# Kernel tuning notes

Hardware: AMD Instinct MI355X
Metric: run time of the kernel (lower is better)

## Reference

```python
import jax, jax.numpy as jnp
import numpy as np

B, S, D = 16, 1024, 1024      # batch, seq_len (== max_ctx_k), input_dim (== embed_dim)
H = 1                          # num_heads (module's v-reshape requires 1)
E = 1024                       # embed_dim
TEMP = 1.0
EPS = 1e-12


def setup_inputs() -> dict:
    key = jax.random.key(0)
    ks = jax.random.split(key, 10)
    x = jax.random.normal(ks[0], (B, S, D), dtype=jnp.float32)
    mask = jax.random.randint(ks[1], (B, S, S), 0, 2, dtype=jnp.int32)
    # parameters (xavier-ish scales)
    Wqkv = jax.random.normal(ks[2], (2 * E, D), dtype=jnp.float32) * (1.0 / np.sqrt(D))
    bqkv = jax.random.normal(ks[3], (2 * E,), dtype=jnp.float32) * 0.02
    Wctx = jax.random.normal(ks[4], (2 * S, S), dtype=jnp.float32) * (1.0 / np.sqrt(S))
    bctx = jax.random.normal(ks[5], (2 * S,), dtype=jnp.float32) * 0.02
    Wf = jax.random.normal(ks[6], (1, 2), dtype=jnp.float32)
    bf = jax.random.normal(ks[7], (1,), dtype=jnp.float32) * 0.02
    Wo = jax.random.normal(ks[8], (D, 2 * D), dtype=jnp.float32) * (1.0 / np.sqrt(2 * D))
    bo = jax.random.normal(ks[9], (D,), dtype=jnp.float32) * 0.02
    return {"x": x, "mask": mask, "Wqkv": Wqkv, "bqkv": bqkv, "Wctx": Wctx,
            "bctx": bctx, "Wf": Wf, "bf": bf, "Wo": Wo, "bo": bo}


def reference(x, mask, Wqkv, bqkv, Wctx, bctx, Wf, bf, Wo, bo):
    head_dim = E // H
    # qkv projection -> (B, H, S, 2*head_dim)
    qkv = (jnp.einsum('bsd,ed->bse', x, Wqkv) + bqkv)
    qkv = qkv.reshape(B, S, H, 2 * head_dim).transpose(0, 2, 1, 3)
    q, k = jnp.split(qkv, 2, axis=-1)
    # v is just x per head (num_heads == 1)
    v = x.reshape(B, S, H, D).transpose(0, 2, 1, 3)          # (B, H, S, D)
    # self-attention scores (NOT scaled by sqrt(d_k), faithful to source)
    self_attn = jnp.einsum('bhqd,bhkd->bhqk', q, k)           # (B, H, S, S)
    # adjacency-derived context scores
    adj = jnp.einsum('bqd,bkd->bqk', x, x)[:, None]           # (B, 1, S, S)
    ctx_qk = jnp.einsum('bhqs,ts->bhqt', adj, Wctx) + bctx    # (B, 1, S, 2S)
    ctx_q, ctx_k = jnp.split(ctx_qk, 2, axis=-1)
    ctx_q = ctx_q / jnp.maximum(jnp.linalg.norm(ctx_q, axis=-1, keepdims=True), EPS)
    ctx_k = ctx_k / jnp.maximum(jnp.linalg.norm(ctx_k, axis=-1, keepdims=True), EPS)
    ctx_attn = jnp.einsum('bhqs,bhks->bhqk', ctx_q, ctx_k)    # (B, 1, S, S)
    # learned fuse of the two score maps: Linear(2 -> 1)
    attn = self_attn * Wf[0, 0] + ctx_attn * Wf[0, 1] + bf[0]
    attn = jax.nn.softmax(attn / TEMP, axis=-1)
    # post-softmax masking + L1 renorm
    m = (mask[:, None] != 0)                                  # (B, 1, S, S)
    attn = jnp.where(m, attn, 0.0)
    attn = attn / jnp.maximum(jnp.sum(jnp.abs(attn), axis=-1, keepdims=True), EPS)
    # value matmul and output projection
    values = jnp.einsum('bhqk,bhkd->bhqd', attn, v)           # (B, H, S, D)
    values = values.transpose(0, 2, 1, 3).reshape(B, S, D)
    o = jnp.einsum('bse,de->bsd', jnp.concatenate([x, values], axis=-1), Wo) + bo
    return o
```

## Files before the change

kernel.cpp:

```cpp
#include <hip/hip_runtime.h>
#include <hip/hip_bf16.h>

#define BB 16
#define SS 1024
#define DD 1024

typedef __hip_bfloat16 bf;
using s8v   = __attribute__((ext_vector_type(8))) short;
using f32x4 = __attribute__((ext_vector_type(4))) float;
using u16x4 = __attribute__((ext_vector_type(4))) unsigned short;
using u16x8 = __attribute__((ext_vector_type(8))) unsigned short;
using i32x4 = __attribute__((ext_vector_type(4))) int;

__device__ __forceinline__ void gload16(const bf* g, unsigned short* l)
{
    __builtin_amdgcn_global_load_lds(
        (const __attribute__((address_space(1))) void*)g,
        (__attribute__((address_space(3))) void*)l,
        16, 0, 0);
}

template <int EP>
__global__ __launch_bounds__(512, 2) void gemm256(
    const bf* __restrict__ A, long sA, int lda, int segA,
    const bf* __restrict__ B, long sB, int ldb, int segB,
    float* __restrict__ C, bf* __restrict__ Cb,
    bf* __restrict__ qp, bf* __restrict__ kp,
    long sC, int ldc, int K,
    const float* __restrict__ bias,
    const float* __restrict__ alpha_ptr, int alpha_idx,
    const float* __restrict__ addc_ptr,
    int accumulate)
{
    __shared__ __align__(16) unsigned short lds[65536];
    unsigned short* Asm = lds;
    unsigned short* Bsm = lds + 32768;

    const int gx = gridDim.x, gy = gridDim.y;
    const int nwg = gx * gy * (int)gridDim.z;
    int lid = blockIdx.x + gx * (blockIdx.y + gy * blockIdx.z);
    lid = (lid & 7) * (nwg >> 3) + (lid >> 3);
    const int bx = lid % gx;
    const int rem = lid / gx;
    const int by = rem % gy;
    const int bz = rem / gy;

    const int tid = threadIdx.x;
    const int w = tid >> 6, l = tid & 63;
    const int wm = w >> 2, wn = w & 3;
    const int lm = l & 15, quad = l >> 4;
    const int bh = wn >> 1;
    const int bl0 = (wn & 1) * 64;

    const int m0 = by * 256, n0 = bx * 256;
    const bf* Ab = A + (long)bz * sA;
    const bf* Bb = B + (long)bz * sB;

    const int srow = w * 16 + (l >> 3);
    const int scol = ((l & 7) ^ (l >> 3)) << 3;
    const long aoff0 = (long)srow * lda + scol;
    const long aoff1 = (long)(srow + 8) * lda + scol;
    const long boff0 = (long)srow * ldb + scol;
    const long boff1 = (long)(srow + 8) * ldb + scol;
    const int ldst = w * 1024;

    auto stageA = [&](int tt, int h) {
        const int kk = ((tt & 15) << 6) +
                       ((((unsigned)segA >> ((tt >> 4) << 3)) & 0xffu) << 10);
        const bf* g = Ab + (long)(m0 + h * 128) * lda + kk;
        unsigned short* d = Asm + (((tt & 1) << 1) + h) * 8192 + ldst;
        gload16(g + aoff0, d);
        gload16(g + aoff1, d + 512);
    };
    auto stageB = [&](int tt, int h) {
        const int kk = ((tt & 15) << 6) +
                       ((((unsigned)segB >> ((tt >> 4) << 3)) & 0xffu) << 10);
        const bf* g = Bb + (long)(n0 + h * 128) * ldb + kk;
        unsigned short* d = Bsm + (((tt & 1) << 1) + h) * 8192 + ldst;
        gload16(g + boff0, d);
        gload16(g + boff1, d + 512);
    };
    auto rdA = [&](int d, int rl, int ks) -> s8v {
        const int off = rl * 64 + (((ks << 5) + (quad << 3)) ^ ((rl & 7) << 3));
        return *(const s8v*)(Asm + ((d << 1) + wm) * 8192 + off);
    };
    auto rdB = [&](int d, int bl, int ks) -> s8v {
        const int off = bl * 64 + (((ks << 5) + (quad << 3)) ^ ((bl & 7) << 3));
        return *(const s8v*)(Bsm + ((d << 1) + bh) * 8192 + off);
    };

    f32x4 acc[8][4];
#pragma unroll
    for (int i = 0; i < 8; ++i)
#pragma unroll
        for (int j = 0; j < 4; ++j)
            acc[i][j] = (f32x4){0.f, 0.f, 0.f, 0.f};

    const int NT = K >> 6;

    stageA(0, 0); stageA(0, 1); stageB(0, 0); stageB(0, 1);
    asm volatile("s_waitcnt vmcnt(4)" ::: "memory");
    stageA(1, 0); stageA(1, 1); stageB(1, 0);
    asm volatile("s_waitcnt vmcnt(6)" ::: "memory");
    __builtin_amdgcn_s_barrier();

    s8v a[8], b[4];
    for (int t = 0; t < NT; ++t) {
        const int d = t & 1;
#pragma unroll
        for (int mf = 0; mf < 4; ++mf) {
            a[mf * 2]     = rdA(d, mf * 16 + lm, 0);
            a[mf * 2 + 1] = rdA(d, mf * 16 + lm, 1);
        }
#pragma unroll
        for (int nf = 0; nf < 2; ++nf) {
            b[nf * 2]     = rdB(d, bl0 + nf * 16 + lm, 0);
            b[nf * 2 + 1] = rdB(d, bl0 + nf * 16 + lm, 1);
        }
        if (t + 1 < NT) stageB(t + 1, 1);
        __builtin_amdgcn_s_barrier();
        __builtin_amdgcn_s_setprio(1);
#pragma unroll
        for (int mf = 0; mf < 4; ++mf)
#pragma unroll
            for (int nf = 0; nf < 2; ++nf) {
                acc[mf][nf] = __builtin_amdgcn_mfma_f32_16x16x32_bf16(a[mf*2],   b[nf*2],   acc[mf][nf], 0, 0, 0);
                acc[mf][nf] = __builtin_amdgcn_mfma_f32_16x16x32_bf16(a[mf*2+1], b[nf*2+1], acc[mf][nf], 0, 0, 0);
            }
        __builtin_amdgcn_s_setprio(0);
        __builtin_amdgcn_s_barrier();
#pragma unroll
        for (int nf = 0; nf < 2; ++nf) {
            b[nf * 2]     = rdB(d, bl0 + (nf + 2) * 16 + lm, 0);
            b[nf * 2 + 1] = rdB(d, bl0 + (nf + 2) * 16 + lm, 1);
        }
        __builtin_amdgcn_s_barrier();
        __builtin_amdgcn_s_setprio(1);
#pragma unroll
        for (int mf = 0; mf < 4; ++mf)
#pragma unroll
            for (int nf = 0; nf < 2; ++nf) {
                acc[mf][nf+2] = __builtin_amdgcn_mfma_f32_16x16x32_bf16(a[mf*2],   b[nf*2],   acc[mf][nf+2], 0, 0, 0);
                acc[mf][nf+2] = __builtin_amdgcn_mfma_f32_16x16x32_bf16(a[mf*2+1], b[nf*2+1], acc[mf][nf+2], 0, 0, 0);
            }
        __builtin_amdgcn_s_setprio(0);
        __builtin_amdgcn_s_barrier();
#pragma unroll
        for (int mf = 0; mf < 4; ++mf) {
            a[mf * 2]     = rdA(d, 64 + mf * 16 + lm, 0);
            a[mf * 2 + 1] = rdA(d, 64 + mf * 16 + lm, 1);
        }
        if (t + 2 < NT) { stageA(t + 2, 0); stageA(t + 2, 1); }
        __builtin_amdgcn_s_barrier();
        __builtin_amdgcn_s_setprio(1);
#pragma unroll
        for (int mf = 0; mf < 4; ++mf)
#pragma unroll
            for (int nf = 0; nf < 2; ++nf) {
                acc[mf+4][nf+2] = __builtin_amdgcn_mfma_f32_16x16x32_bf16(a[mf*2],   b[nf*2],   acc[mf+4][nf+2], 0, 0, 0);
                acc[mf+4][nf+2] = __builtin_amdgcn_mfma_f32_16x16x32_bf16(a[mf*2+1], b[nf*2+1], acc[mf+4][nf+2], 0, 0, 0);
            }
        __builtin_amdgcn_s_setprio(0);
        __builtin_amdgcn_s_barrier();
#pragma unroll
        for (int nf = 0; nf < 2; ++nf) {
            b[nf * 2]     = rdB(d, bl0 + nf * 16 + lm, 0);
            b[nf * 2 + 1] = rdB(d, bl0 + nf * 16 + lm, 1);
        }
        if (t + 2 < NT) {
            stageB(t + 2, 0);
            asm volatile("s_waitcnt vmcnt(6)" ::: "memory");
        } else {
            asm volatile("s_waitcnt vmcnt(0)" ::: "memory");
        }
        __builtin_amdgcn_s_barrier();
        __builtin_amdgcn_s_setprio(1);
#pragma unroll
        for (int mf = 0; mf < 4; ++mf)
#pragma unroll
            for (int nf = 0; nf < 2; ++nf) {
                acc[mf+4][nf] = __builtin_amdgcn_mfma_f32_16x16x32_bf16(a[mf*2],   b[nf*2],   acc[mf+4][nf], 0, 0, 0);
                acc[mf+4][nf] = __builtin_amdgcn_mfma_f32_16x16x32_bf16(a[mf*2+1], b[nf*2+1], acc[mf+4][nf], 0, 0, 0);
            }
        __builtin_amdgcn_s_setprio(0);
        __builtin_amdgcn_s_barrier();
    }

    const float alpha = alpha_ptr ? alpha_ptr[alpha_idx] : 1.0f;
    const float addc  = addc_ptr ? addc_ptr[0] : 0.0f;
    float* Cp = C ? C + (long)bz * sC : nullptr;
    bf* Cbp = (EP == 1) ? Cb + (long)bz * sC : nullptr;
    bf* qpz = (EP == 2 || EP == 3) ? qp + (long)bz * sC : nullptr;
    bf* kpz = (EP == 2 || EP == 3) ? kp + (long)bz * sC : nullptr;

#pragma unroll
    for (int mf = 0; mf < 8; ++mf) {
#pragma unroll
        for (int nf = 0; nf < 4; ++nf) {
            const int cidx = n0 + wn * 64 + nf * 16 + lm;
            const float bv = bias ? bias[cidx] : 0.0f;
            const long rbase = m0 + wm * 128 + mf * 16 + quad * 4;
#pragma unroll
            for (int r = 0; r < 4; ++r) {
                const long row = rbase + r;
                if (EP == 2) {
                    float v = acc[mf][nf][r] + bv;
                    if (cidx < 1024) {
                        v *= alpha;
                        bf hi = __float2bfloat16(v);
                        bf lo = __float2bfloat16(v - __bfloat162float(hi));
                        qpz[row * 3072 + cidx] = hi;
                        qpz[row * 3072 + 1024 + cidx] = lo;
                    } else {
                        const int c = cidx - 1024;
                        bf hi = __float2bfloat16(v);
                        bf lo = __float2bfloat16(v - __bfloat162float(hi));
                        kpz[row * 3072 + c] = hi;
                        kpz[row * 3072 + 1024 + c] = lo;
                    }
                } else if (EP == 3) {
                    const float v = acc[mf][nf][r] + bv;
                    const bf h = __float2bfloat16(v);
                    if (cidx < 1024) qpz[row * 3072 + 2048 + cidx] = h;
                    else             kpz[row * 3072 + 2048 + (cidx - 1024)] = h;
                } else {
                    float v = alpha * acc[mf][nf][r] + addc + bv;
                    const long off = row * (long)ldc + cidx;
                    if (EP == 1) {
                        Cbp[off] = __float2bfloat16(v);
                    } else {
                        if (accumulate) v += Cp[off];
                        Cp[off] = v;
                    }
                }
            }
        }
    }
}

__device__ inline float blockReduceSum(float v, float* red)
{
#pragma unroll
    for (int off = 32; off > 0; off >>= 1) v += __shfl_xor(v, off, 64);
    __syncthreads();
    if ((threadIdx.x & 63) == 0) red[threadIdx.x >> 6] = v;
    __syncthreads();
    return red[0] + red[1] + red[2] + red[3];
}

__device__ inline float blockReduceMax(float v, float* red)
{
#pragma unroll
    for (int off = 32; off > 0; off >>= 1) v = fmaxf(v, __shfl_xor(v, off, 64));
    __syncthreads();
    if ((threadIdx.x & 63) == 0) red[threadIdx.x >> 6] = v;
    __syncthreads();
    return fmaxf(fmaxf(red[0], red[1]), fmaxf(red[2], red[3]));
}

__device__ inline void split_bf16(float v, bf& hi, bf& lo)
{
    hi = __float2bfloat16(v);
    lo = __float2bfloat16(v - __bfloat162float(hi));
}

__device__ __forceinline__ unsigned short bf_bits(float v)
{
    bf h = __float2bfloat16(v);
    return *reinterpret_cast<unsigned short*>(&h);
}

__global__ __launch_bounds__(256) void prep_wqkv_kernel(
    const float* __restrict__ W, bf* __restrict__ wq2)
{
    const long i4 = ((long)blockIdx.x * 256 + threadIdx.x) * 4;
    const long r = i4 >> 10; const int c = (int)(i4 & 1023);
    const f32x4 s = *(const f32x4*)&W[i4];
    u16x4 h4, l4;
#pragma unroll
    for (int j = 0; j < 4; ++j) {
        bf hi, lo; split_bf16(s[j], hi, lo);
        h4[j] = *reinterpret_cast<unsigned short*>(&hi);
        l4[j] = *reinterpret_cast<unsigned short*>(&lo);
    }
    *(u16x4*)&wq2[r * 2048 + c] = h4;
    *(u16x4*)&wq2[r * 2048 + 1024 + c] = l4;
}

__global__ __launch_bounds__(256) void conv_kernel(
    const float* __restrict__ src, bf* __restrict__ dst, int cols, int src_ld, long n)
{
    const long i4 = ((long)blockIdx.x * 256 + threadIdx.x) * 4;
    if (i4 >= n) return;
    const long r = i4 / cols; const int c = (int)(i4 % cols);
    const f32x4 s = *(const f32x4*)&src[r * src_ld + c];
    u16x4 d4;
#pragma unroll
    for (int j = 0; j < 4; ++j) d4[j] = bf_bits(s[j]);
    *(u16x4*)&dst[i4] = d4;
}

__global__ __launch_bounds__(256) void conv_x_kernel(
    const float* __restrict__ x, bf* __restrict__ xhl, bf* __restrict__ xT1)
{
    __shared__ float t[64][65];
    const int b = blockIdx.z;
    const int c0 = blockIdx.x * 64, r0 = blockIdx.y * 64;
    const int tx = threadIdx.x & 7, ty = threadIdx.x >> 3;
    const float* xb = x + (long)b * SS * DD;
    bf* xhlb = xhl + (long)b * SS * 2048;
#pragma unroll
    for (int p = 0; p < 2; ++p) {
        const int r = ty + 32 * p;
        const f32x4 v0 = *(const f32x4*)&xb[(long)(r0 + r) * DD + c0 + tx * 8];
        const f32x4 v1 = *(const f32x4*)&xb[(long)(r0 + r) * DD + c0 + tx * 8 + 4];
        u16x8 hv, lv;
#pragma unroll
        for (int j = 0; j < 4; ++j) {
            bf hi, lo;
            split_bf16(v0[j], hi, lo);
            hv[j] = *reinterpret_cast<unsigned short*>(&hi);
            lv[j] = *reinterpret_cast<unsigned short*>(&lo);
            t[r][tx * 8 + j] = v0[j];
            split_bf16(v1[j], hi, lo);
            hv[j + 4] = *reinterpret_cast<unsigned short*>(&hi);
            lv[j + 4] = *reinterpret_cast<unsigned short*>(&lo);
            t[r][tx * 8 + 4 + j] = v1[j];
        }
        *(u16x8*)&xhlb[(long)(r0 + r) * 2048 + c0 + tx * 8] = hv;
        *(u16x8*)&xhlb[(long)(r0 + r) * 2048 + 1024 + c0 + tx * 8] = lv;
    }
    __syncthreads();
#pragma unroll
    for (int p = 0; p < 2; ++p) {
        const int dd = ty + 32 * p;
        u16x8 o;
#pragma unroll
        for (int j = 0; j < 8; ++j) o[j] = bf_bits(t[tx * 8 + j][dd]);
        *(u16x8*)&xT1[(long)b * DD * SS + (long)(c0 + dd) * SS + r0 + tx * 8] = o;
    }
}

__global__ __launch_bounds__(256) void l2norm_fuse_kernel(
    bf* __restrict__ q3, bf* __restrict__ k3, const float* __restrict__ Wf)
{
    __shared__ float red[4];
    const long row = blockIdx.x >> 1;
    const int half = blockIdx.x & 1;
    bf* p = (half ? k3 : q3) + row * 3072 + 2048;
    const int t = threadIdx.x;

    const u16x4 u = *reinterpret_cast<const u16x4*>(p + 4 * t);
    float v[4];
    float ss = 0.0f;
#pragma unroll
    for (int i = 0; i < 4; ++i) {
        unsigned short us = u[i];
        v[i] = __bfloat162float(*reinterpret_cast<const bf*>(&us));
        ss = fmaf(v[i], v[i], ss);
    }
    ss = blockReduceSum(ss, red);
    const float inv = 1.0f / fmaxf(sqrtf(ss), 1e-12f);
    const float scale = half ? inv : inv * Wf[1];
    u16x4 o;
#pragma unroll
    for (int i = 0; i < 4; ++i) o[i] = bf_bits(v[i] * scale);
    *reinterpret_cast<u16x4*>(p + 4 * t) = o;
}

__global__ __launch_bounds__(256) void softmax_mask_kernel(
    const float* __restrict__ attn, const int* __restrict__ mask, bf* __restrict__ attn_bf)
{
    __shared__ float red[4];
    const long row = blockIdx.x;
    const int t4 = threadIdx.x * 4;
    const f32x4 v = *(const f32x4*)(attn + row * SS + t4);
    const i32x4 mv = *(const i32x4*)(mask + row * SS + t4);
    bf* o = attn_bf + row * SS;

    float mx = fmaxf(fmaxf(v[0], v[1]), fmaxf(v[2], v[3]));
    mx = blockReduceMax(mx, red);

    float e[4];
    float s = 0.0f;
#pragma unroll
    for (int i = 0; i < 4; ++i) { e[i] = expf(v[i] - mx); s += e[i]; }
    s = blockReduceSum(s, red);

    float l1 = 0.0f;
#pragma unroll
    for (int i = 0; i < 4; ++i) { e[i] = mv[i] ? e[i] / s : 0.0f; l1 += e[i]; }
    l1 = blockReduceSum(l1, red);
    const float inv = 1.0f / fmaxf(l1, 1e-12f);
    u16x4 ov;
#pragma unroll
    for (int i = 0; i < 4; ++i) ov[i] = bf_bits(e[i] * inv);
    *(u16x4*)(o + t4) = ov;
}

extern "C" void kernel_launch(void* const* d_in, const int* in_sizes, int n_in,
                              void* d_out, int out_size, void* d_ws, size_t ws_size,
                              hipStream_t stream)
{
    const float* x    = (const float*)d_in[0];
    const int*   mask = (const int*)d_in[1];
    const float* Wqkv = (const float*)d_in[2];
    const float* bqkv = (const float*)d_in[3];
    const float* Wctx = (const float*)d_in[4];
    const float* bctx = (const float*)d_in[5];
    const float* Wf   = (const float*)d_in[6];
    const float* bfp  = (const float*)d_in[7];
    const float* Wo   = (const float*)d_in[8];
    const float* bo   = (const float*)d_in[9];
    float* out = (float*)d_out;

    const long SD = (long)SS * DD;

    auto align_up = [](size_t v) { return (v + 255) & ~(size_t)255; };

    const size_t sz_wq2  = 2048L * 2048 * 2;
    const size_t sz_wctx = 2048L * 1024 * 2;
    const size_t sz_wob  = 1024L * 2048 * 2;
    const size_t SH = align_up(sz_wq2) + align_up(sz_wctx) + align_up(sz_wob);

    const size_t szXL = 1024L * 2048 * 2;
    const size_t szXT = 1024L * 1024 * 2;
    const size_t szQ3 = 1024L * 3072 * 2;
    const size_t szY  = 1024L * 1024 * 4;
    const size_t PB = align_up(szXL) + align_up(szXT) + 2 * align_up(szQ3) +
                      align_up(szY);

    int G = 16;
    while (G > 1 && SH + (size_t)G * PB > ws_size) G >>= 1;

    char* p = (char*)d_ws;
    auto take = [&](size_t bytes) { char* r = p; p += align_up(bytes); return r; };
    bf* Wq2   = (bf*)take(sz_wq2);
    bf* Wctx1 = (bf*)take(sz_wctx);
    bf* Wob   = (bf*)take(sz_wob);
    char* RX = take((size_t)G * szXL);
    char* RT = take((size_t)G * szXT);
    char* RQ = take((size_t)G * szQ3);
    char* RK = take((size_t)G * szQ3);
    char* RY = take((size_t)G * szY);

    bf*    xhl   = (bf*)RX;
    bf*    xT1   = (bf*)RT;
    bf*    Q3    = (bf*)RQ;
    bf*    K3    = (bf*)RK;
    bf*    adjb  = (bf*)RY;
    float* attn  = (float*)RY;
    bf*    attnb = (bf*)RQ;

    const dim3 blk(256);
    const dim3 blk5(512);
    const long sXL = 1024L * 2048;
    const long sAT = 1024L * 1024;
    const long sQ3 = 1024L * 3072;

    const int segQKV_A = 0x0100;
    const int segQKV_B = 0x010000;
    const int segATT_A = 0x02010000;
    const int segATT_B = 0x02000100;
    const int segOUT   = 0x0100;

    prep_wqkv_kernel<<<dim3((2048L * 1024) / 1024), blk, 0, stream>>>(Wqkv, Wq2);
    conv_kernel<<<dim3((2048L * 1024) / 1024), blk, 0, stream>>>(Wctx, Wctx1, 1024, 1024, 2048L * 1024);
    conv_kernel<<<dim3((1024L * 2048) / 1024), blk, 0, stream>>>(Wo, Wob, 2048, 2048, 1024L * 2048);

    for (int bc0 = 0; bc0 < BB; bc0 += G) {
        const float* xb = x + (long)bc0 * SD;
        const int M = G * 1024;

        conv_x_kernel<<<dim3(16, 16, G), blk, 0, stream>>>(xb, xhl, xT1);

        gemm256<2><<<dim3(2048 / 256, M / 256), blk5, 0, stream>>>(
            xhl, 0, 2048, segQKV_A, Wq2, 0, 2048, segQKV_B,
            nullptr, nullptr, Q3, K3, 0, 0, 3072,
            bqkv, Wf, 0, nullptr, 0);

        gemm256<1><<<dim3(1024 / 256, 1024 / 256, G), blk5, 0, stream>>>(
            xhl, sXL, 2048, 0, xhl, sXL, 2048, 0,
            nullptr, adjb, nullptr, nullptr, sAT, 1024, 1024,
            nullptr, nullptr, 0, nullptr, 0);

        gemm256<3><<<dim3(2048 / 256, 1024 / 256, G), blk5, 0, stream>>>(
            adjb, sAT, 1024, 0, Wctx1, 0, 1024, 0,
            nullptr, nullptr, Q3, K3, sQ3, 0, 1024,
            bctx, nullptr, 0, nullptr, 0);

        l2norm_fuse_kernel<<<dim3(G * 1024 * 2), blk, 0, stream>>>(Q3, K3, Wf);

        gemm256<0><<<dim3(1024 / 256, 1024 / 256, G), blk5, 0, stream>>>(
            Q3, sQ3, 3072, segATT_A, K3, sQ3, 3072, segATT_B,
            attn, nullptr, nullptr, nullptr, sAT, 1024, 4096,
            nullptr, nullptr, 0, bfp, 0);

        softmax_mask_kernel<<<dim3(G * 1024), blk, 0, stream>>>(
            attn, mask + (long)bc0 * SS * SS, attnb);

        gemm256<1><<<dim3(1024 / 256, 1024 / 256, G), blk5, 0, stream>>>(
            attnb, sAT, 1024, 0, xT1, sAT, 1024, 0,
            nullptr, xhl + 1024, nullptr, nullptr, sXL, 2048, 1024,
            nullptr, nullptr, 0, nullptr, 0);

        gemm256<0><<<dim3(1024 / 256, M / 256), blk5, 0, stream>>>(
            xhl, 0, 2048, segOUT, Wob, 0, 2048, segOUT,
            out + (long)bc0 * SD, nullptr, nullptr, nullptr, 0, 1024, 2048,
            bo, nullptr, 0, nullptr, 0);
    }
}
```

Baseline: 1.004 ms.

## Load GEMM B fragments directly from global into registers, halving LDS use

The B operand is no longer staged through shared memory. Each wave loads its own B fragments straight from global memory into double-buffered registers (bA/bB), and the tile loop is restructured into two unrolled halves with fewer barriers. This removes the LDS traffic and synchronisation for B and halves the shared-memory footprint, which could allow more occupancy. In exchange, every wave re-reads B from global or L2 with no sharing across waves, and register pressure rises from holding 16 extra B vectors.

```diff
diff --git a/kernel.cpp b/kernel.cpp
--- a/kernel.cpp
+++ b/kernel.cpp
@@ -32,9 +32,7 @@
     const float* __restrict__ addc_ptr,
     int accumulate)
 {
-    __shared__ __align__(16) unsigned short lds[65536];
-    unsigned short* Asm = lds;
-    unsigned short* Bsm = lds + 32768;
+    __shared__ __align__(16) unsigned short Asm[32768];
 
     const int gx = gridDim.x, gy = gridDim.y;
     const int nwg = gx * gy * (int)gridDim.z;
@@ -49,8 +47,6 @@
     const int w = tid >> 6, l = tid & 63;
     const int wm = w >> 2, wn = w & 3;
     const int lm = l & 15, quad = l >> 4;
-    const int bh = wn >> 1;
-    const int bl0 = (wn & 1) * 64;
 
     const int m0 = by * 256, n0 = bx * 256;
     const bf* Ab = A + (long)bz * sA;
@@ -60,8 +56,6 @@
     const int scol = ((l & 7) ^ (l >> 3)) << 3;
     const long aoff0 = (long)srow * lda + scol;
     const long aoff1 = (long)(srow + 8) * lda + scol;
-    const long boff0 = (long)srow * ldb + scol;
-    const long boff1 = (long)(srow + 8) * ldb + scol;
     const int ldst = w * 1024;
 
     auto stageA = [&](int tt, int h) {
@@ -72,21 +66,20 @@
         gload16(g + aoff0, d);
         gload16(g + aoff1, d + 512);
     };
-    auto stageB = [&](int tt, int h) {
-        const int kk = ((tt & 15) << 6) +
-                       ((((unsigned)segB >> ((tt >> 4) << 3)) & 0xffu) << 10);
-        const bf* g = Bb + (long)(n0 + h * 128) * ldb + kk;
-        unsigned short* d = Bsm + (((tt & 1) << 1) + h) * 8192 + ldst;
-        gload16(g + boff0, d);
-        gload16(g + boff1, d + 512);
-    };
     auto rdA = [&](int d, int rl, int ks) -> s8v {
         const int off = rl * 64 + (((ks << 5) + (quad << 3)) ^ ((rl & 7) << 3));
         return *(const s8v*)(Asm + ((d << 1) + wm) * 8192 + off);
     };
-    auto rdB = [&](int d, int bl, int ks) -> s8v {
-        const int off = bl * 64 + (((ks << 5) + (quad << 3)) ^ ((bl & 7) << 3));
-        return *(const s8v*)(Bsm + ((d << 1) + bh) * 8192 + off);
+    const bf* Bw = Bb + (long)(n0 + wn * 64 + lm) * ldb + quad * 8;
+    auto loadB = [&](int tt, s8v* dst) {
+        const int kk = ((tt & 15) << 6) +
+                       ((((unsigned)segB >> ((tt >> 4) << 3)) & 0xffu) << 10);
+#pragma unroll
+        for (int nf = 0; nf < 4; ++nf)
+#pragma unroll
+            for (int ks = 0; ks < 2; ++ks)
+                dst[nf * 2 + ks] =
+                    *(const s8v*)&Bw[(long)(nf * 16) * ldb + kk + ks * 32];
     };
 
     f32x4 acc[8][4];
@@ -97,51 +90,30 @@
             acc[i][j] = (f32x4){0.f, 0.f, 0.f, 0.f};
 
     const int NT = K >> 6;
-
-    stageA(0, 0); stageA(0, 1); stageB(0, 0); stageB(0, 1);
-    asm volatile("s_waitcnt vmcnt(4)" ::: "memory");
-    stageA(1, 0); stageA(1, 1); stageB(1, 0);
-    asm volatile("s_waitcnt vmcnt(6)" ::: "memory");
+    s8v bA[8], bB[8];
+
+    stageA(0, 0); stageA(0, 1);
+    loadB(0, bA);
+    stageA(1, 0); stageA(1, 1);
+    asm volatile("s_waitcnt vmcnt(12)" ::: "memory");
     __builtin_amdgcn_s_barrier();
 
-    s8v a[8], b[4];
-    for (int t = 0; t < NT; ++t) {
+    auto tile = [&](int t, s8v* bc, s8v* bn) {
         const int d = t & 1;
+        s8v a[8];
 #pragma unroll
         for (int mf = 0; mf < 4; ++mf) {
             a[mf * 2]     = rdA(d, mf * 16 + lm, 0);
             a[mf * 2 + 1] = rdA(d, mf * 16 + lm, 1);
         }
-#pragma unroll
-        for (int nf = 0; nf < 2; ++nf) {
-            b[nf * 2]     = rdB(d, bl0 + nf * 16 + lm, 0);
-            b[nf * 2 + 1] = rdB(d, bl0 + nf * 16 + lm, 1);
-        }
-        if (t + 1 < NT) stageB(t + 1, 1);
-        __builtin_amdgcn_s_barrier();
+        if (t + 1 < NT) loadB(t + 1, bn);
         __builtin_amdgcn_s_setprio(1);
 #pragma unroll
         for (int mf = 0; mf < 4; ++mf)
 #pragma unroll
-            for (int nf = 0; nf < 2; ++nf) {
-                acc[mf][nf] = __builtin_amdgcn_mfma_f32_16x16x32_bf16(a[mf*2],   b[nf*2],   acc[mf][nf], 0, 0, 0);
-                acc[mf][nf] = __builtin_amdgcn_mfma_f32_16x16x32_bf16(a[mf*2+1], b[nf*2+1], acc[mf][nf], 0, 0, 0);
-            }
-        __builtin_amdgcn_s_setprio(0);
-        __builtin_amdgcn_s_barrier();
-#pragma unroll
-        for (int nf = 0; nf < 2; ++nf) {
-            b[nf * 2]     = rdB(d, bl0 + (nf + 2) * 16 + lm, 0);
-            b[nf * 2 + 1] = rdB(d, bl0 + (nf + 2) * 16 + lm, 1);
-        }
-        __builtin_amdgcn_s_barrier();
-        __builtin_amdgcn_s_setprio(1);
-#pragma unroll
-        for (int mf = 0; mf < 4; ++mf)
-#pragma unroll
-            for (int nf = 0; nf < 2; ++nf) {
-                acc[mf][nf+2] = __builtin_amdgcn_mfma_f32_16x16x32_bf16(a[mf*2],   b[nf*2],   acc[mf][nf+2], 0, 0, 0);
-                acc[mf][nf+2] = __builtin_amdgcn_mfma_f32_16x16x32_bf16(a[mf*2+1], b[nf*2+1], acc[mf][nf+2], 0, 0, 0);
+            for (int nf = 0; nf < 4; ++nf) {
+                acc[mf][nf] = __builtin_amdgcn_mfma_f32_16x16x32_bf16(a[mf*2],   bc[nf*2],   acc[mf][nf], 0, 0, 0);
+                acc[mf][nf] = __builtin_amdgcn_mfma_f32_16x16x32_bf16(a[mf*2+1], bc[nf*2+1], acc[mf][nf], 0, 0, 0);
             }
         __builtin_amdgcn_s_setprio(0);
         __builtin_amdgcn_s_barrier();
@@ -151,39 +123,27 @@
             a[mf * 2 + 1] = rdA(d, 64 + mf * 16 + lm, 1);
         }
         if (t + 2 < NT) { stageA(t + 2, 0); stageA(t + 2, 1); }
-        __builtin_amdgcn_s_barrier();
         __builtin_amdgcn_s_setprio(1);
 #pragma unroll
         for (int mf = 0; mf < 4; ++mf)
 #pragma unroll
-            for (int nf = 0; nf < 2; ++nf) {
-                acc[mf+4][nf+2] = __builtin_amdgcn_mfma_f32_16x16x32_bf16(a[mf*2],   b[nf*2],   acc[mf+4][nf+2], 0, 0, 0);
-                acc[mf+4][nf+2] = __builtin_amdgcn_mfma_f32_16x16x32_bf16(a[mf*2+1], b[nf*2+1], acc[mf+4][nf+2], 0, 0, 0);
+            for (int nf = 0; nf < 4; ++nf) {
+                acc[mf+4][nf] = __builtin_amdgcn_mfma_f32_16x16x32_bf16(a[mf*2],   bc[nf*2],   acc[mf+4][nf], 0, 0, 0);
+                acc[mf+4][nf] = __builtin_amdgcn_mfma_f32_16x16x32_bf16(a[mf*2+1], bc[nf*2+1], acc[mf+4][nf], 0, 0, 0);
             }
         __builtin_amdgcn_s_setprio(0);
-        __builtin_amdgcn_s_barrier();
-#pragma unroll
-        for (int nf = 0; nf < 2; ++nf) {
-            b[nf * 2]     = rdB(d, bl0 + nf * 16 + lm, 0);
-            b[nf * 2 + 1] = rdB(d, bl0 + nf * 16 + lm, 1);
+        if (t + 1 < NT) {
+            if (t + 2 < NT)
+                asm volatile("s_waitcnt vmcnt(12)" ::: "memory");
+            else
+                asm volatile("s_waitcnt vmcnt(8)" ::: "memory");
+            __builtin_amdgcn_s_barrier();
         }
-        if (t + 2 < NT) {
-            stageB(t + 2, 0);
-            asm volatile("s_waitcnt vmcnt(6)" ::: "memory");
-        } else {
-            asm volatile("s_waitcnt vmcnt(0)" ::: "memory");
-        }
-        __builtin_amdgcn_s_barrier();
-        __builtin_amdgcn_s_setprio(1);
-#pragma unroll
-        for (int mf = 0; mf < 4; ++mf)
-#pragma unroll
-            for (int nf = 0; nf < 2; ++nf) {
-                acc[mf+4][nf] = __builtin_amdgcn_mfma_f32_16x16x32_bf16(a[mf*2],   b[nf*2],   acc[mf+4][nf], 0, 0, 0);
-                acc[mf+4][nf] = __builtin_amdgcn_mfma_f32_16x16x32_bf16(a[mf*2+1], b[nf*2+1], acc[mf+4][nf], 0, 0, 0);
-            }
-        __builtin_amdgcn_s_setprio(0);
-        __builtin_amdgcn_s_barrier();
+    };
+
+    for (int t = 0; t < NT; t += 2) {
+        tile(t, bA, bB);
+        tile(t + 1, bB, bA);
     }
 
     const float alpha = alpha_ptr ? alpha_ptr[alpha_idx] : 1.0f;
```

New measurement: 1.356 ms. +35.1%, slower.
